# Kernel optimization log

Measured on AMD Instinct MI355X. Metric: run time of the kernel, lower is better.

The kernel has to match this reference:

```python
import jax, jax.numpy as jnp
import numpy as np

N, L, E, NB, H = 128, 200, 128, 2, 2
ITEM = 50000
TEMP = 0.2
HD = E // H


def _ln(x, g, b, eps=1e-8):
    m = x.mean(-1, keepdims=True)
    v = ((x - m) ** 2).mean(-1, keepdims=True)
    return (x - m) / jnp.sqrt(v + eps) * g + b


def setup_inputs() -> dict:
    key = jax.random.key(0)
    ks = jax.random.split(key, 20)
    rng = np.random.default_rng(0)
    log_seqs = rng.integers(1, ITEM + 1, size=(N, L))
    lens = rng.integers(20, L + 1, size=(N,))
    log_seqs[np.arange(L)[None, :] < (L - lens[:, None])] = 0  # left padding, id 0
    pos_seqs = rng.integers(1, ITEM + 1, size=(N, L))
    neg_seqs = rng.integers(1, ITEM + 1, size=(N, L))
    item_emb = jax.random.normal(ks[0], (ITEM + 1, E), jnp.float32) * 0.02
    item_emb = item_emb.at[0].set(0.0)  # padding_idx=0
    s = 1.0 / np.sqrt(E)
    return {
        "item_emb": item_emb,
        "pos_emb": jax.random.normal(ks[1], (L + 1, E), jnp.float32) * 0.02,
        "W_asp": jax.random.normal(ks[2], (16, E, E), jnp.float32) * s,
        "w_weight": jax.random.normal(ks[3], (2 * E,), jnp.float32) * (1.0 / np.sqrt(2 * E)),
        "w_bias": jnp.zeros((), jnp.float32),
        "attn_ln_g": jnp.ones((NB, E), jnp.float32),
        "attn_ln_b": jnp.zeros((NB, E), jnp.float32),
        "in_proj_w": jax.random.normal(ks[4], (NB, 3 * E, E), jnp.float32) * s,
        "in_proj_b": jnp.zeros((NB, 3 * E), jnp.float32),
        "out_proj_w": jax.random.normal(ks[5], (NB, E, E), jnp.float32) * s,
        "out_proj_b": jnp.zeros((NB, E), jnp.float32),
        "fwd_ln_g": jnp.ones((NB, E), jnp.float32),
        "fwd_ln_b": jnp.zeros((NB, E), jnp.float32),
        "conv1_w": jax.random.normal(ks[6], (NB, E, E), jnp.float32) * s,
        "conv1_b": jnp.zeros((NB, E), jnp.float32),
        "conv2_w": jax.random.normal(ks[7], (NB, E, E), jnp.float32) * s,
        "conv2_b": jnp.zeros((NB, E), jnp.float32),
        "last_ln_g": jnp.ones((E,), jnp.float32),
        "last_ln_b": jnp.zeros((E,), jnp.float32),
        "user_ids": jnp.asarray(rng.integers(0, 100000, size=(N,)), jnp.int32),
        "log_seqs": jnp.asarray(log_seqs, jnp.int32),
        "pos_seqs": jnp.asarray(pos_seqs, jnp.int32),
        "neg_seqs": jnp.asarray(neg_seqs, jnp.int32),
        "epoch": 1,
    }


def reference(item_emb, pos_emb, W_asp, w_weight, w_bias, attn_ln_g, attn_ln_b,
              in_proj_w, in_proj_b, out_proj_w, out_proj_b, fwd_ln_g, fwd_ln_b,
              conv1_w, conv1_b, conv2_w, conv2_b, last_ln_g, last_ln_b,
              user_ids, log_seqs, pos_seqs, neg_seqs, epoch):
    tmask = (log_seqs == 0)                               # (N,L) True=pad
    validL = (~tmask).astype(item_emb.dtype)              # (N,L)
    seqs0 = item_emb[log_seqs] * validL[..., None]
    pos_embs = item_emb[pos_seqs] * validL[..., None]
    neg_embs = item_emb[neg_seqs] * validL[..., None]

    validE = jnp.concatenate([validL, validL[:, -1:]], 1)  # (N,L+1)
    kv_save = jnp.concatenate([seqs0, pos_embs[:, -1:, :]], 1)  # (N,L+1,E)

    def aspects(x, valid, residual):
        a = jnp.einsum('nli,aoi->nlao', x, W_asp)          # 16 expert GEMMs batched
        if residual:
            a = a + x[:, :, None, :]
            a = a / (jnp.linalg.norm(a, axis=-1, keepdims=True) + 1e-8)
        return a * valid[:, :, None, None]

    kv4 = aspects(kv_save, validE, True)                   # (N,L+1,16,E)
    temp = aspects(kv_save, validE, False)
    nvalid = validE.sum()
    cent_loss = jnp.linalg.norm(kv_save * validE[..., None] - temp.mean(2), axis=-1).sum() / nvalid

    norm_x = kv4 / (jnp.linalg.norm(kv4, axis=-1, keepdims=True) + 1e-8)
    pos_s = (norm_x * norm_x).sum(-1)                      # (N,L+1,16)
    ttl = jnp.einsum('nlae,nlbe->nlab', norm_x, norm_x)    # pairwise cosine sims
    mi = -(pos_s / TEMP - jnp.log(jnp.exp(ttl / TEMP).sum(-1)))
    ind_loss = (mi * validE[:, :, None]).sum() / nvalid

    s = kv4.sum(2)                                         # (N,L+1,E)
    q = jnp.cumsum(s, 1) - s                               # exclusive cumsum
    cnt = jnp.cumsum(validE, 1) - validE
    q = q / (16.0 * cnt + 1e-8)[..., None] * validE[..., None]

    w_q, w_a = w_weight[:E], w_weight[E:]

    def gate(qv, a4):                                      # learned softmax gating
        logits = (qv @ w_q)[:, :, None] + a4 @ w_a + w_bias
        w = jax.nn.softmax(logits, axis=2)
        return (a4 * w[..., None]).sum(2)

    re_all = gate(q, kv4)                                  # (N,L+1,E)
    re_emb = re_all[:, :L] + kv4[:, :L].mean(2)

    neg_kv4 = aspects(neg_embs, validL, True)
    q2 = q[:, 1:, :] * validL[..., None]
    neg_t = gate(q2, neg_kv4) + neg_kv4.mean(2)
    pos_t = re_all[:, 1:, :] * validL[..., None] + (kv4[:, 1:] * validL[..., None, None]).mean(2)

    seqs = re_emb * (E ** 0.5) + pos_emb[jnp.arange(L)][None]
    seqs = seqs * validL[..., None]
    causal = jnp.where(jnp.tril(jnp.ones((L, L), bool)), 0.0, -1e9)
    scale = HD ** -0.5
    for i in range(NB):
        Qn = _ln(seqs, attn_ln_g[i], attn_ln_b[i])
        qp = Qn @ in_proj_w[i][:E].T + in_proj_b[i][:E]
        kp = seqs @ in_proj_w[i][E:2 * E].T + in_proj_b[i][E:2 * E]
        vp = seqs @ in_proj_w[i][2 * E:].T + in_proj_b[i][2 * E:]
        sp = lambda x: x.reshape(N, L, H, HD).transpose(0, 2, 1, 3)
        att = jax.nn.softmax(jnp.einsum('nhqd,nhkd->nhqk', sp(qp), sp(kp)) * scale + causal, axis=-1)
        o = jnp.einsum('nhqk,nhkd->nhqd', att, sp(vp)).transpose(0, 2, 1, 3).reshape(N, L, E)
        seqs = Qn + (o @ out_proj_w[i].T + out_proj_b[i])
        seqs = _ln(seqs, fwd_ln_g[i], fwd_ln_b[i])
        h = jax.nn.relu(seqs @ conv1_w[i].T + conv1_b[i])
        seqs = (h @ conv2_w[i].T + conv2_b[i]) + seqs
        seqs = seqs * validL[..., None]
    log_feats = _ln(seqs, last_ln_g, last_ln_b)
    pos_logits = (log_feats * pos_t).sum(-1)
    neg_logits = (log_feats * neg_t).sum(-1)
    return (pos_logits, neg_logits, ind_loss, cent_loss)
```

## Files before the change

### kernel.cpp

```cpp
#include <hip/hip_runtime.h>
#include <hip/hip_bf16.h>
#include <cstddef>

typedef __attribute__((ext_vector_type(8))) short bf16x8;
typedef __attribute__((ext_vector_type(4))) float f32x4;
typedef unsigned short ushort_t;

__device__ __forceinline__ short f2bf(float f) {
    __hip_bfloat16 h = __float2bfloat16(f);
    return __builtin_bit_cast(short, h);
}
__device__ __forceinline__ float bf2f(short s) {
    unsigned u = ((unsigned)(unsigned short)s) << 16;
    return __builtin_bit_cast(float, u);
}
__device__ __forceinline__ unsigned pk2(float a, float b) {
    return (unsigned)(unsigned short)f2bf(a) | ((unsigned)(unsigned short)f2bf(b) << 16);
}

__global__ void cvt_all(const float* __restrict__ s0, const float* __restrict__ s1,
                        const float* __restrict__ s2, const float* __restrict__ s3,
                        const float* __restrict__ s4, ushort_t* __restrict__ dst) {
    const int i = blockIdx.x * 256 + threadIdx.x;
    const int mat = i >> 14;
    const int wm = i & 16383;
    const int blk = wm >> 9;
    const int t = blk >> 2, f = blk & 3;
    const int lane = (wm >> 3) & 63;
    const int j = wm & 7;
    const int g4 = lane >> 4, nn = lane & 15;
    const int srcoff = (t * 16 + nn) * 128 + f * 32 + g4 * 8 + j;
    const float* src; int mbase;
    if (mat < 16)      { src = s0; mbase = mat; }
    else if (mat < 22) { src = s1; mbase = mat - 16; }
    else if (mat < 24) { src = s2; mbase = mat - 22; }
    else if (mat < 26) { src = s3; mbase = mat - 24; }
    else               { src = s4; mbase = mat - 26; }
    dst[i] = (ushort_t)f2bf(src[(size_t)mbase * 16384 + srcoff]);
}

__global__ void gather_kernel(const float* __restrict__ item_emb,
                              const int* __restrict__ log_seqs,
                              const int* __restrict__ pos_seqs,
                              const int* __restrict__ neg_seqs,
                              ushort_t* __restrict__ kvx, ushort_t* __restrict__ negx,
                              float* __restrict__ validE, float* __restrict__ validL) {
    const int r = blockIdx.x;
    const int e = threadIdx.x;
    const int NKV = 128 * 201;
    if (r < NKV) {
        const int n = r / 201, l = r % 201;
        float vl; int sidx;
        if (l < 200) { sidx = log_seqs[n * 200 + l]; vl = (sidx != 0) ? 1.f : 0.f; }
        else { vl = (log_seqs[n * 200 + 199] != 0) ? 1.f : 0.f; sidx = pos_seqs[n * 200 + 199]; }
        kvx[(size_t)r * 128 + e] = (ushort_t)f2bf(item_emb[(size_t)sidx * 128 + e] * vl);
        if (e == 0) validE[r] = vl;
    } else {
        const int rr = r - NKV;
        const int n = rr / 200, l = rr % 200;
        const float vl = (log_seqs[n * 200 + l] != 0) ? 1.f : 0.f;
        const int sidx = neg_seqs[n * 200 + l];
        negx[(size_t)rr * 128 + e] = (ushort_t)f2bf(item_emb[(size_t)sidx * 128 + e] * vl);
        if (e == 0) validL[rr] = vl;
    }
}

__global__ __launch_bounds__(512, 1) void aspects2_kernel(
        const ushort_t* __restrict__ X, const ushort_t* __restrict__ Wab,
        const float* __restrict__ w_weight, const float* __restrict__ validf,
        float* __restrict__ Gout, float* __restrict__ pInd, float* __restrict__ pCent,
        int nLossBlocks) {
    __shared__ ushort_t rsb[32 * 2184];
    __shared__ ushort_t xsb[32 * 136];
    __shared__ float wal[128];
    __shared__ float s_red[512];
    __shared__ float s_lg[512];
    __shared__ float s_pos[512];
    __shared__ float vld[32];
    __shared__ float centw[32];
    __shared__ float miw[32];

    const int tid = threadIdx.x;
    const int row0 = blockIdx.x * 32;
    const bool losses = (int)blockIdx.x < nLossBlocks;
    const int lane = tid & 63, w = tid >> 6;
    const int g4 = lane >> 4, nn = lane & 15;

    {
        const int r = tid >> 4, c8 = (tid & 15) * 8;
        *(int4*)&xsb[r * 136 + c8] = *(const int4*)&X[(size_t)(row0 + r) * 128 + c8];
    }
    if (tid < 128) wal[tid] = w_weight[128 + tid];
    if (tid < 32) vld[tid] = validf[row0 + tid];
    __syncthreads();

    bf16x8 xf0[4], xf1[4];
#pragma unroll
    for (int f = 0; f < 4; ++f) {
        xf0[f] = *(const bf16x8*)&xsb[nn * 136 + f * 32 + g4 * 8];
        xf1[f] = *(const bf16x8*)&xsb[(nn + 16) * 136 + f * 32 + g4 * 8];
    }

    for (int al = 0; al < 2; ++al) {
        const int a = w * 2 + al;
        const ushort_t* wbase = Wab + (size_t)a * 16384 + lane * 8;
        float np0 = 0.f, lp0 = 0.f, np1 = 0.f, lp1 = 0.f;
#pragma unroll
        for (int t = 0; t < 8; ++t) {
            f32x4 d0 = {0.f, 0.f, 0.f, 0.f}, d1 = d0;
#pragma unroll
            for (int f = 0; f < 4; ++f) {
                bf16x8 wf = *(const bf16x8*)&wbase[(t * 4 + f) * 512];
                d0 = __builtin_amdgcn_mfma_f32_16x16x32_bf16(wf, xf0[f], d0, 0, 0, 0);
                d1 = __builtin_amdgcn_mfma_f32_16x16x32_bf16(wf, xf1[f], d1, 0, 0, 0);
            }
            const int o0 = t * 16 + g4 * 4;
            const float4 wv = *(const float4*)&wal[o0];
            const int xs0 = o0 & 4;
            {
                const bf16x8 xb = *(const bf16x8*)&xsb[nn * 136 + (o0 & ~7)];
                const float v0 = d0[0] + bf2f(xb[xs0]);
                const float v1 = d0[1] + bf2f(xb[xs0 + 1]);
                const float v2 = d0[2] + bf2f(xb[xs0 + 2]);
                const float v3 = d0[3] + bf2f(xb[xs0 + 3]);
                np0 += v0 * v0 + v1 * v1 + v2 * v2 + v3 * v3;
                lp0 += v0 * wv.x + v1 * wv.y + v2 * wv.z + v3 * wv.w;
                *(int2*)&rsb[nn * 2184 + a * 136 + o0] =
                    make_int2((int)pk2(v0, v1), (int)pk2(v2, v3));
            }
            {
                const bf16x8 xb = *(const bf16x8*)&xsb[(nn + 16) * 136 + (o0 & ~7)];
                const float v0 = d1[0] + bf2f(xb[xs0]);
                const float v1 = d1[1] + bf2f(xb[xs0 + 1]);
                const float v2 = d1[2] + bf2f(xb[xs0 + 2]);
                const float v3 = d1[3] + bf2f(xb[xs0 + 3]);
                np1 += v0 * v0 + v1 * v1 + v2 * v2 + v3 * v3;
                lp1 += v0 * wv.x + v1 * wv.y + v2 * wv.z + v3 * wv.w;
                *(int2*)&rsb[(nn + 16) * 2184 + a * 136 + o0] =
                    make_int2((int)pk2(v0, v1), (int)pk2(v2, v3));
            }
        }
        np0 += __shfl_xor(np0, 16, 64); np0 += __shfl_xor(np0, 32, 64);
        lp0 += __shfl_xor(lp0, 16, 64); lp0 += __shfl_xor(lp0, 32, 64);
        np1 += __shfl_xor(np1, 16, 64); np1 += __shfl_xor(np1, 32, 64);
        lp1 += __shfl_xor(lp1, 16, 64); lp1 += __shfl_xor(lp1, 32, 64);
        if (lane < 16) {
            s_red[nn * 16 + a] = np0;        s_lg[nn * 16 + a] = lp0;
            s_red[(nn + 16) * 16 + a] = np1; s_lg[(nn + 16) * 16 + a] = lp1;
        }
    }
    __syncthreads();

    {
        const float nrm = sqrtf(s_red[tid]);
        const float inv1 = 1.f / (nrm + 1e-8f);
        const float n2 = nrm * inv1;
        const float sg = inv1 / (n2 + 1e-8f);
        const float ts = n2 / (n2 + 1e-8f);
        const float logit = s_lg[tid] * inv1;
        float mx = logit;
#pragma unroll
        for (int m = 1; m < 16; m <<= 1) mx = fmaxf(mx, __shfl_xor(mx, m, 16));
        const float e = __expf(logit - mx);
        float ssum = e;
#pragma unroll
        for (int m = 1; m < 16; m <<= 1) ssum += __shfl_xor(ssum, m, 16);
        s_red[tid] = sg;
        s_pos[tid] = ts * ts * 5.f;
        s_lg[tid] = (e / ssum + 0.0625f) * inv1;
    }
    __syncthreads();

    {
        const int row = tid >> 4, ol = tid & 15, o8 = ol * 8;
        float g[8] = {0.f, 0.f, 0.f, 0.f, 0.f, 0.f, 0.f, 0.f};
        float sr[8] = {0.f, 0.f, 0.f, 0.f, 0.f, 0.f, 0.f, 0.f};
#pragma unroll
        for (int a = 0; a < 16; ++a) {
            const bf16x8 vb = *(const bf16x8*)&rsb[row * 2184 + a * 136 + o8];
            const float gw = s_lg[row * 16 + a];
#pragma unroll
            for (int j = 0; j < 8; ++j) {
                const float v = bf2f(vb[j]);
                g[j] += v * gw;
                if (losses) sr[j] += v;
            }
        }
        float* go = &Gout[(size_t)(row0 + row) * 128 + o8];
        *(float4*)go       = make_float4(g[0], g[1], g[2], g[3]);
        *(float4*)(go + 4) = make_float4(g[4], g[5], g[6], g[7]);
        if (losses) {
            const bf16x8 xb = *(const bf16x8*)&xsb[row * 136 + o8];
            float c = 0.f;
#pragma unroll
            for (int j = 0; j < 8; ++j) {
                const float dd = 2.f * bf2f(xb[j]) - sr[j] * 0.0625f;
                c += dd * dd;
            }
            c += __shfl_xor(c, 1, 64);
            c += __shfl_xor(c, 2, 64);
            c += __shfl_xor(c, 4, 64);
            c += __shfl_xor(c, 8, 64);
            if (ol == 0) centw[row] = sqrtf(c) * vld[row];
        }
    }

    if (losses) {
        for (int rl = 0; rl < 4; ++rl) {
            const int row = w * 4 + rl;
            f32x4 dd = {0.f, 0.f, 0.f, 0.f};
#pragma unroll
            for (int f = 0; f < 4; ++f) {
                bf16x8 fr = *(const bf16x8*)&rsb[row * 2184 + nn * 136 + f * 32 + g4 * 8];
                dd = __builtin_amdgcn_mfma_f32_16x16x32_bf16(fr, fr, dd, 0, 0, 0);
            }
            const float sgb = s_red[row * 16 + nn];
            float mis = 0.f;
#pragma unroll
            for (int r = 0; r < 4; ++r) {
                const int a = g4 * 4 + r;
                const float sga = s_red[row * 16 + a];
                float eb = __expf(5.f * dd[r] * sga * sgb);
#pragma unroll
                for (int m = 1; m < 16; m <<= 1) eb += __shfl_xor(eb, m, 16);
                mis += -(s_pos[row * 16 + a] - logf(eb));
            }
            mis += __shfl_xor(mis, 16, 64);
            mis += __shfl_xor(mis, 32, 64);
            if (lane == 0) miw[row] = mis * vld[row];
        }
        __syncthreads();
        if (tid == 0) {
            float si = 0.f, sc = 0.f;
#pragma unroll
            for (int r = 0; r < 32; ++r) { si += miw[r]; sc += centw[r]; }
            pInd[blockIdx.x] = si;
            pCent[blockIdx.x] = sc;
        }
    }
}

__global__ __launch_bounds__(256) void qkv_kernel(const float* __restrict__ X,
                                                  const ushort_t* __restrict__ W3,
                                                  const float* __restrict__ b3,
                                                  const float* __restrict__ lng,
                                                  const float* __restrict__ lnb,
                                                  float* __restrict__ Xn,
                                                  ushort_t* __restrict__ qo,
                                                  ushort_t* __restrict__ ko,
                                                  ushort_t* __restrict__ vo) {
    const int tid = threadIdx.x, lane = tid & 63, w = tid >> 6;
    const int q = lane >> 4, nn = lane & 15;
    const int m0 = blockIdx.x * 64 + w * 16;
    float xv[4][8];
    float s = 0.f, sq = 0.f;
    const float* xr = &X[(size_t)(m0 + nn) * 128];
#pragma unroll
    for (int f = 0; f < 4; ++f) {
        const float4 a = *(const float4*)&xr[f * 32 + q * 8];
        const float4 b = *(const float4*)&xr[f * 32 + q * 8 + 4];
        xv[f][0] = a.x; xv[f][1] = a.y; xv[f][2] = a.z; xv[f][3] = a.w;
        xv[f][4] = b.x; xv[f][5] = b.y; xv[f][6] = b.z; xv[f][7] = b.w;
        s += (a.x + a.y) + (a.z + a.w) + (b.x + b.y) + (b.z + b.w);
        sq += (a.x * a.x + a.y * a.y) + (a.z * a.z + a.w * a.w)
            + (b.x * b.x + b.y * b.y) + (b.z * b.z + b.w * b.w);
    }
    bf16x8 afr[4];
#pragma unroll
    for (int f = 0; f < 4; ++f) {
        bf16x8 v;
#pragma unroll
        for (int j = 0; j < 8; ++j) v[j] = f2bf(xv[f][j]);
        afr[f] = v;
    }
    s += __shfl_xor(s, 16, 64);  s += __shfl_xor(s, 32, 64);
    sq += __shfl_xor(sq, 16, 64); sq += __shfl_xor(sq, 32, 64);
    const float mean = s * 0.0078125f;
    const float var = fmaxf(sq * 0.0078125f - mean * mean, 0.f);
    const float inv = rsqrtf(var + 1e-8f);
    bf16x8 afq[4];
#pragma unroll
    for (int f = 0; f < 4; ++f) {
        const int c0 = f * 32 + q * 8;
        const float4 ga = *(const float4*)&lng[c0];
        const float4 gb = *(const float4*)&lng[c0 + 4];
        const float4 ba = *(const float4*)&lnb[c0];
        const float4 bb = *(const float4*)&lnb[c0 + 4];
        float y[8];
        y[0] = (xv[f][0] - mean) * inv * ga.x + ba.x;
        y[1] = (xv[f][1] - mean) * inv * ga.y + ba.y;
        y[2] = (xv[f][2] - mean) * inv * ga.z + ba.z;
        y[3] = (xv[f][3] - mean) * inv * ga.w + ba.w;
        y[4] = (xv[f][4] - mean) * inv * gb.x + bb.x;
        y[5] = (xv[f][5] - mean) * inv * gb.y + bb.y;
        y[6] = (xv[f][6] - mean) * inv * gb.z + bb.z;
        y[7] = (xv[f][7] - mean) * inv * gb.w + bb.w;
        float* xo = &Xn[(size_t)(m0 + nn) * 128 + c0];
        *(float4*)xo       = make_float4(y[0], y[1], y[2], y[3]);
        *(float4*)(xo + 4) = make_float4(y[4], y[5], y[6], y[7]);
        bf16x8 v;
#pragma unroll
        for (int j = 0; j < 8; ++j) v[j] = f2bf(y[j]);
        afq[f] = v;
    }
    ushort_t* const outs[3] = {qo, ko, vo};
#pragma unroll
    for (int mi = 0; mi < 3; ++mi) {
        const ushort_t* wbase = W3 + (size_t)mi * 16384 + lane * 8;
        f32x4 acc[8];
#pragma unroll
        for (int t = 0; t < 8; ++t) acc[t] = (f32x4){0.f, 0.f, 0.f, 0.f};
#pragma unroll
        for (int t = 0; t < 8; ++t) {
#pragma unroll
            for (int f = 0; f < 4; ++f) {
                bf16x8 b = *(const bf16x8*)&wbase[(t * 4 + f) * 512];
                acc[t] = __builtin_amdgcn_mfma_f32_16x16x32_bf16(
                    (mi == 0) ? afq[f] : afr[f], b, acc[t], 0, 0, 0);
            }
        }
        const float* bi = b3 + mi * 128;
        ushort_t* outp = outs[mi];
#pragma unroll
        for (int t = 0; t < 8; ++t) {
            const int n = t * 16 + nn;
            const float bv = bi[n];
#pragma unroll
            for (int r = 0; r < 4; ++r) {
                const int row = m0 + q * 4 + r;
                outp[(size_t)row * 128 + n] = (ushort_t)f2bf(acc[t][r] + bv);
            }
        }
    }
}

__global__ __launch_bounds__(256) void ffn_kernel(const ushort_t* __restrict__ attno,
                                                  const ushort_t* __restrict__ outWb,
                                                  const float* __restrict__ outB,
                                                  const float* __restrict__ resQn,
                                                  const float* __restrict__ lng,
                                                  const float* __restrict__ lnb,
                                                  const ushort_t* __restrict__ c1wb,
                                                  const float* __restrict__ c1b,
                                                  const ushort_t* __restrict__ c2wb,
                                                  const float* __restrict__ c2b,
                                                  const float* __restrict__ validL,
                                                  float* __restrict__ seqs) {
    __shared__ ushort_t hls[64 * 136];
    const int tid = threadIdx.x, lane = tid & 63, w = tid >> 6;
    const int q = lane >> 4, nn = lane & 15;
    const int m0 = blockIdx.x * 64 + w * 16;
    const int wrow = w * 16;

    bf16x8 af[4];
    {
        const ushort_t* xb = &attno[(size_t)(m0 + nn) * 128];
#pragma unroll
        for (int f = 0; f < 4; ++f) af[f] = *(const bf16x8*)&xb[f * 32 + q * 8];
    }
    f32x4 acc[8];
#pragma unroll
    for (int t = 0; t < 8; ++t) acc[t] = (f32x4){0.f, 0.f, 0.f, 0.f};
    {
        const ushort_t* wbase = outWb + lane * 8;
#pragma unroll
        for (int t = 0; t < 8; ++t)
#pragma unroll
            for (int f = 0; f < 4; ++f) {
                bf16x8 b = *(const bf16x8*)&wbase[(t * 4 + f) * 512];
                acc[t] = __builtin_amdgcn_mfma_f32_16x16x32_bf16(af[f], b, acc[t], 0, 0, 0);
            }
    }
    float y[8][4];
    float s[4] = {0.f, 0.f, 0.f, 0.f}, sq[4] = {0.f, 0.f, 0.f, 0.f};
#pragma unroll
    for (int t = 0; t < 8; ++t) {
        const int n = t * 16 + nn;
        const float bi = outB[n];
#pragma unroll
        for (int r = 0; r < 4; ++r) {
            const float v = acc[t][r] + bi + resQn[(size_t)(m0 + q * 4 + r) * 128 + n];
            y[t][r] = v;
            s[r] += v;
            sq[r] += v * v;
        }
    }
#pragma unroll
    for (int m = 1; m < 16; m <<= 1) {
#pragma unroll
        for (int r = 0; r < 4; ++r) {
            s[r] += __shfl_xor(s[r], m, 64);
            sq[r] += __shfl_xor(sq[r], m, 64);
        }
    }
#pragma unroll
    for (int r = 0; r < 4; ++r) {
        const float mean = s[r] * 0.0078125f;
        const float var = fmaxf(sq[r] * 0.0078125f - mean * mean, 0.f);
        const float inv = rsqrtf(var + 1e-8f);
        s[r] = mean; sq[r] = inv;
    }
#pragma unroll
    for (int t = 0; t < 8; ++t) {
        const int n = t * 16 + nn;
        const float g = lng[n], b = lnb[n];
#pragma unroll
        for (int r = 0; r < 4; ++r) {
            const float v = (y[t][r] - s[r]) * sq[r] * g + b;
            y[t][r] = v;
            hls[(wrow + q * 4 + r) * 136 + n] = (ushort_t)f2bf(v);
        }
    }
    __syncthreads();
    {
        const ushort_t* xb = &hls[(wrow + nn) * 136];
#pragma unroll
        for (int f = 0; f < 4; ++f) af[f] = *(const bf16x8*)&xb[f * 32 + q * 8];
    }
    f32x4 acc2[8];
#pragma unroll
    for (int t = 0; t < 8; ++t) acc2[t] = (f32x4){0.f, 0.f, 0.f, 0.f};
    {
        const ushort_t* wbase = c1wb + lane * 8;
#pragma unroll
        for (int t = 0; t < 8; ++t)
#pragma unroll
            for (int f = 0; f < 4; ++f) {
                bf16x8 b = *(const bf16x8*)&wbase[(t * 4 + f) * 512];
                acc2[t] = __builtin_amdgcn_mfma_f32_16x16x32_bf16(af[f], b, acc2[t], 0, 0, 0);
            }
    }
    __syncthreads();
#pragma unroll
    for (int t = 0; t < 8; ++t) {
        const int n = t * 16 + nn;
        const float bi = c1b[n];
#pragma unroll
        for (int r = 0; r < 4; ++r)
            hls[(wrow + q * 4 + r) * 136 + n] = (ushort_t)f2bf(fmaxf(acc2[t][r] + bi, 0.f));
    }
    __syncthreads();
    {
        const ushort_t* xb = &hls[(wrow + nn) * 136];
#pragma unroll
        for (int f = 0; f < 4; ++f) af[f] = *(const bf16x8*)&xb[f * 32 + q * 8];
    }
    f32x4 acc3[8];
#pragma unroll
    for (int t = 0; t < 8; ++t) acc3[t] = (f32x4){0.f, 0.f, 0.f, 0.f};
    {
        const ushort_t* wbase = c2wb + lane * 8;
#pragma unroll
        for (int t = 0; t < 8; ++t)
#pragma unroll
            for (int f = 0; f < 4; ++f) {
                bf16x8 b = *(const bf16x8*)&wbase[(t * 4 + f) * 512];
                acc3[t] = __builtin_amdgcn_mfma_f32_16x16x32_bf16(af[f], b, acc3[t], 0, 0, 0);
            }
    }
    float mk[4];
#pragma unroll
    for (int r = 0; r < 4; ++r) mk[r] = validL[m0 + q * 4 + r];
#pragma unroll
    for (int t = 0; t < 8; ++t) {
        const int n = t * 16 + nn;
        const float bi = c2b[n];
#pragma unroll
        for (int r = 0; r < 4; ++r) {
            const int row = m0 + q * 4 + r;
            seqs[(size_t)row * 128 + n] = (acc3[t][r] + bi + y[t][r]) * mk[r];
        }
    }
}

__global__ void reduce_kernel(const float* __restrict__ pInd, const float* __restrict__ pCent,
                              int nblk, const float* __restrict__ validE, int nve,
                              float* __restrict__ outp) {
    __shared__ float a1[256], a2[256], a3[256];
    const int tid = threadIdx.x;
    float si = 0.f, sc = 0.f, nv = 0.f;
    for (int t = tid; t < nblk; t += 256) { si += pInd[t]; sc += pCent[t]; }
    for (int t = tid; t < nve; t += 256) nv += validE[t];
    a1[tid] = si; a2[tid] = sc; a3[tid] = nv;
    __syncthreads();
    for (int s = 128; s > 0; s >>= 1) {
        if (tid < s) { a1[tid] += a1[tid + s]; a2[tid] += a2[tid + s]; a3[tid] += a3[tid + s]; }
        __syncthreads();
    }
    if (tid == 0) { outp[0] = a1[0] / a3[0]; outp[1] = a2[0] / a3[0]; }
}

__global__ void seqs_init(const float* __restrict__ G, const float* __restrict__ pos_emb,
                          const float* __restrict__ validL, float* __restrict__ seqs) {
    const int idx = blockIdx.x * 256 + threadIdx.x;
    const int e = idx & 127;
    const int nl = idx >> 7;
    const int l = nl % 200, n = nl / 200;
    const float v = G[((size_t)n * 201 + l) * 128 + e] * 11.313708498984761f + pos_emb[l * 128 + e];
    seqs[idx] = v * validL[nl];
}

__global__ __launch_bounds__(256) void attn_kernel(const ushort_t* __restrict__ qp,
                                                   const ushort_t* __restrict__ kp,
                                                   const ushort_t* __restrict__ vp,
                                                   ushort_t* __restrict__ outp) {
    __shared__ ushort_t KsU[2048];
    __shared__ ushort_t VtU[2560];
    __shared__ ushort_t Pb[2560];

    const int tid = threadIdx.x, lane = tid & 63, w = tid >> 6;
    const int b = blockIdx.x;
    const int nh = b >> 2, qt = b & 3;
    const int n = nh >> 1, h = nh & 1;
    const size_t base = (size_t)n * 200 * 128 + (size_t)h * 64;
    const int qw = qt * 64 + w * 16;
    const bool wactive = qw < 200;
    const int q15 = lane & 15, g4 = lane >> 4;
    const int qglob = qw + q15;

    bf16x8 qf[2];
    {
        const int qr = (qglob < 200) ? qglob : 199;
#pragma unroll
        for (int f = 0; f < 2; ++f)
            qf[f] = *(const bf16x8*)&qp[base + (size_t)qr * 128 + f * 32 + g4 * 8];
    }
    f32x4 Oacc[4];
#pragma unroll
    for (int nt = 0; nt < 4; ++nt) Oacc[nt] = (f32x4){0.f, 0.f, 0.f, 0.f};
    float mrun = -1e30f, lrun = 0.f;

    const int kmax = min(200, qt * 64 + 64);
    ushort_t* PbW = Pb + w * 640;

    for (int jt = 0; jt < kmax; jt += 32) {
        __syncthreads();
        {
            const int k = tid >> 3, e0 = (tid & 7) * 8;
            const int krow = jt + k;
            int4 a = make_int4(0, 0, 0, 0);
            if (krow < 200) a = *(const int4*)&kp[base + (size_t)krow * 128 + e0];
            *(int4*)&KsU[(k * 128 + ((e0 * 2) ^ ((k & 7) << 4))) >> 1] = a;
        }
        {
            const int k = tid & 31, e0 = (tid >> 5) * 8;
            const int vrow = jt + k;
            int4 a = make_int4(0, 0, 0, 0);
            if (vrow < 200) a = *(const int4*)&vp[base + (size_t)vrow * 128 + e0];
            VtU[(e0 + 0) * 40 + k] = (ushort_t)((unsigned)a.x & 0xFFFF);
            VtU[(e0 + 1) * 40 + k] = (ushort_t)((unsigned)a.x >> 16);
            VtU[(e0 + 2) * 40 + k] = (ushort_t)((unsigned)a.y & 0xFFFF);
            VtU[(e0 + 3) * 40 + k] = (ushort_t)((unsigned)a.y >> 16);
            VtU[(e0 + 4) * 40 + k] = (ushort_t)((unsigned)a.z & 0xFFFF);
            VtU[(e0 + 5) * 40 + k] = (ushort_t)((unsigned)a.z >> 16);
            VtU[(e0 + 6) * 40 + k] = (ushort_t)((unsigned)a.w & 0xFFFF);
            VtU[(e0 + 7) * 40 + k] = (ushort_t)((unsigned)a.w >> 16);
        }
        __syncthreads();
        if (!wactive) continue;

        f32x4 d0 = {0.f, 0.f, 0.f, 0.f}, d1 = d0;
#pragma unroll
        for (int f = 0; f < 2; ++f) {
            const int ebyte = g4 * 16 + f * 64;
            const int sw = ebyte ^ ((q15 & 7) << 4);
            bf16x8 a0 = *(const bf16x8*)&KsU[(q15 * 128 + sw) >> 1];
            bf16x8 a1 = *(const bf16x8*)&KsU[((q15 + 16) * 128 + sw) >> 1];
            d0 = __builtin_amdgcn_mfma_f32_16x16x32_bf16(a0, qf[f], d0, 0, 0, 0);
            d1 = __builtin_amdgcn_mfma_f32_16x16x32_bf16(a1, qf[f], d1, 0, 0, 0);
        }
        const int kb = jt + g4 * 4;
        float p[8];
        float tmax = -1e30f;
#pragma unroll
        for (int r = 0; r < 4; ++r) {
            const float s0 = (kb + r      <= qglob) ? d0[r] * 0.125f : -1e30f;
            const float s1 = (kb + r + 16 <= qglob) ? d1[r] * 0.125f : -1e30f;
            p[r] = s0; p[r + 4] = s1;
            tmax = fmaxf(tmax, fmaxf(s0, s1));
        }
        tmax = fmaxf(tmax, __shfl_xor(tmax, 16, 64));
        tmax = fmaxf(tmax, __shfl_xor(tmax, 32, 64));
        const float mnew = fmaxf(mrun, tmax);
        const float corr = __expf(mrun - mnew);
        mrun = mnew;
        float tsum = 0.f;
#pragma unroll
        for (int i = 0; i < 8; ++i) {
            float pe = __expf(p[i] - mnew);
            pe = bf2f(f2bf(pe));
            p[i] = pe;
            tsum += pe;
        }
        tsum += __shfl_xor(tsum, 16, 64);
        tsum += __shfl_xor(tsum, 32, 64);
        lrun = lrun * corr + tsum;
        const int kl = g4 * 4;
        *(unsigned*)&PbW[q15 * 40 + kl]          = pk2(p[0], p[1]);
        *(unsigned*)&PbW[q15 * 40 + kl + 2]      = pk2(p[2], p[3]);
        *(unsigned*)&PbW[q15 * 40 + 16 + kl]     = pk2(p[4], p[5]);
        *(unsigned*)&PbW[q15 * 40 + 16 + kl + 2] = pk2(p[6], p[7]);
        asm volatile("" ::: "memory");
        float corr_r[4];
#pragma unroll
        for (int r = 0; r < 4; ++r) corr_r[r] = __shfl(corr, g4 * 4 + r, 64);
#pragma unroll
        for (int nt = 0; nt < 4; ++nt) {
#pragma unroll
            for (int r = 0; r < 4; ++r) Oacc[nt][r] *= corr_r[r];
        }
        bf16x8 pa = *(const bf16x8*)&PbW[q15 * 40 + g4 * 8];
#pragma unroll
        for (int nt = 0; nt < 4; ++nt) {
            bf16x8 vb = *(const bf16x8*)&VtU[(nt * 16 + q15) * 40 + g4 * 8];
            Oacc[nt] = __builtin_amdgcn_mfma_f32_16x16x32_bf16(pa, vb, Oacc[nt], 0, 0, 0);
        }
    }
    if (wactive) {
        float linv[4];
#pragma unroll
        for (int r = 0; r < 4; ++r) linv[r] = 1.f / __shfl(lrun, g4 * 4 + r, 64);
#pragma unroll
        for (int r = 0; r < 4; ++r) {
            const int qg = qw + g4 * 4 + r;
            if (qg < 200) {
#pragma unroll
                for (int nt = 0; nt < 4; ++nt)
                    outp[base + (size_t)qg * 128 + nt * 16 + q15] =
                        (ushort_t)f2bf(Oacc[nt][r] * linv[r]);
            }
        }
    }
}

__global__ __launch_bounds__(256) void logits_kernel(const float* __restrict__ seqs,
                                                     const float* __restrict__ lastg,
                                                     const float* __restrict__ lastb,
                                                     const float* __restrict__ G,
                                                     const float* __restrict__ negt,
                                                     const float* __restrict__ validL,
                                                     float* __restrict__ outp) {
    const int row = blockIdx.x * 4 + (threadIdx.x >> 6);
    const int lane = threadIdx.x & 63;
    if (row >= 25600) return;
    const int n = row / 200, j = row % 200;
    const float2 x = *(const float2*)&seqs[(size_t)row * 128 + lane * 2];
    float s = x.x + x.y, sq = x.x * x.x + x.y * x.y;
#pragma unroll
    for (int m = 1; m < 64; m <<= 1) { s += __shfl_xor(s, m, 64); sq += __shfl_xor(sq, m, 64); }
    const float mean = s * 0.0078125f;
    const float var = fmaxf(sq * 0.0078125f - mean * mean, 0.f);
    const float inv = rsqrtf(var + 1e-8f);
    const float2 gg = *(const float2*)&lastg[lane * 2];
    const float2 bb = *(const float2*)&lastb[lane * 2];
    const float y0 = (x.x - mean) * inv * gg.x + bb.x;
    const float y1 = (x.y - mean) * inv * gg.y + bb.y;
    const float2 g2 = *(const float2*)&G[((size_t)n * 201 + j + 1) * 128 + lane * 2];
    const float2 t2 = *(const float2*)&negt[(size_t)row * 128 + lane * 2];
    float sp = y0 * g2.x + y1 * g2.y;
    float sn = y0 * t2.x + y1 * t2.y;
#pragma unroll
    for (int m = 1; m < 64; m <<= 1) { sp += __shfl_xor(sp, m, 64); sn += __shfl_xor(sn, m, 64); }
    if (lane == 0) { outp[row] = sp * validL[row]; outp[25600 + row] = sn; }
}

extern "C" void kernel_launch(void* const* d_in, const int* in_sizes, int n_in,
                              void* d_out, int out_size, void* d_ws, size_t ws_size,
                              hipStream_t stream) {
    (void)in_sizes; (void)n_in; (void)out_size; (void)ws_size;
    const float* item_emb = (const float*)d_in[0];
    const float* pos_emb  = (const float*)d_in[1];
    const float* W_asp    = (const float*)d_in[2];
    const float* w_weight = (const float*)d_in[3];
    const float* attn_g = (const float*)d_in[5];
    const float* attn_b = (const float*)d_in[6];
    const float* inW    = (const float*)d_in[7];
    const float* inB    = (const float*)d_in[8];
    const float* outW   = (const float*)d_in[9];
    const float* outB   = (const float*)d_in[10];
    const float* fwd_g  = (const float*)d_in[11];
    const float* fwd_b  = (const float*)d_in[12];
    const float* c1w    = (const float*)d_in[13];
    const float* c1b    = (const float*)d_in[14];
    const float* c2w    = (const float*)d_in[15];
    const float* c2b    = (const float*)d_in[16];
    const float* last_g = (const float*)d_in[17];
    const float* last_b = (const float*)d_in[18];
    const int* log_seqs = (const int*)d_in[20];
    const int* pos_seqs = (const int*)d_in[21];
    const int* neg_seqs = (const int*)d_in[22];

    float* ws = (float*)d_ws;
    const size_t S = (size_t)128 * 201 * 128;
    ushort_t* kvx  = (ushort_t*)ws;
    ushort_t* negx = kvx + S;
    ushort_t* qp = (ushort_t*)ws;
    ushort_t* kp = qp + (size_t)25600 * 128;
    float* G     = ws + 2 * S;
    float* negt  = ws + 3 * S;
    float* seqs  = ws + 4 * S;
    float* Qn    = ws + 5 * S;
    ushort_t* vp    = (ushort_t*)(ws + 6 * S);
    ushort_t* attno = (ushort_t*)(ws + 7 * S);
    ushort_t* wb  = (ushort_t*)(ws + 8 * S);
    ushort_t* Wab  = wb;
    ushort_t* inWb = Wab + 262144;
    ushort_t* outWb = inWb + 98304;
    ushort_t* c1b_w = outWb + 32768;
    ushort_t* c2b_w = c1b_w + 32768;
    float* validE = ws + 8 * S + 229376;
    float* validL = validE + 128 * 201;
    float* pInd   = validL + 128 * 200;
    float* pCent  = pInd + 804;
    float* outF   = (float*)d_out;

    cvt_all<<<dim3(1792), dim3(256), 0, stream>>>(W_asp, inW, outW, c1w, c2w, wb);
    gather_kernel<<<dim3(128 * 201 + 128 * 200), dim3(128), 0, stream>>>(
        item_emb, log_seqs, pos_seqs, neg_seqs, kvx, negx, validE, validL);
    aspects2_kernel<<<dim3(1604), dim3(512), 0, stream>>>(
        kvx, Wab, w_weight, validE, G, pInd, pCent, 804);
    reduce_kernel<<<dim3(1), dim3(256), 0, stream>>>(
        pInd, pCent, 804, validE, 128 * 201, outF + 51200);
    seqs_init<<<dim3(12800), dim3(256), 0, stream>>>(G, pos_emb, validL, seqs);

    for (int i = 0; i < 2; ++i) {
        qkv_kernel<<<dim3(400), dim3(256), 0, stream>>>(
            seqs, inWb + (size_t)i * 3 * 16384, inB + (size_t)i * 384,
            attn_g + i * 128, attn_b + i * 128, Qn, qp, kp, vp);
        attn_kernel<<<dim3(1024), dim3(256), 0, stream>>>(qp, kp, vp, attno);
        ffn_kernel<<<dim3(400), dim3(256), 0, stream>>>(
            attno, outWb + (size_t)i * 16384, outB + i * 128, Qn,
            fwd_g + i * 128, fwd_b + i * 128,
            c1b_w + (size_t)i * 16384, c1b + i * 128,
            c2b_w + (size_t)i * 16384, c2b + i * 128,
            validL, seqs);
    }
    logits_kernel<<<dim3(6400), dim3(256), 0, stream>>>(
        seqs, last_g, last_b, G, negt, validL, outF);
}
```

Measured before the change: 243.9 us.

## Fuse seqs init into aspects kernel and compute norms/logits via MFMA Gram

Removes the separate seqs_init launch by writing the scaled G plus positional embedding directly from the aspects kernel for the loss blocks, which cover the KV rows. Replaces the per-thread norm and logit accumulation in the aspect loop with an MFMA pass over the stored bf16 aspect results: the Gram diagonal gives the norms and a product with bf16 w_weight gives the logits. The Gram is then reused for the later MI loss instead of being recomputed. This cuts one kernel launch and a global read/write of seqs, but norms and logits are now computed from bf16-rounded values.

Result: faster. 232.0 us (-4.9%).

```diff
diff --git a/kernel.cpp b/kernel.cpp
--- a/kernel.cpp
+++ b/kernel.cpp
@@ -68,11 +68,13 @@
 __global__ __launch_bounds__(512, 1) void aspects2_kernel(
         const ushort_t* __restrict__ X, const ushort_t* __restrict__ Wab,
         const float* __restrict__ w_weight, const float* __restrict__ validf,
-        float* __restrict__ Gout, float* __restrict__ pInd, float* __restrict__ pCent,
+        const float* __restrict__ pos_emb,
+        float* __restrict__ Gout, float* __restrict__ seqs,
+        float* __restrict__ pInd, float* __restrict__ pCent,
         int nLossBlocks) {
     __shared__ ushort_t rsb[32 * 2184];
     __shared__ ushort_t xsb[32 * 136];
-    __shared__ float wal[128];
+    __shared__ ushort_t wal_b[128];
     __shared__ float s_red[512];
     __shared__ float s_lg[512];
     __shared__ float s_pos[512];
@@ -90,21 +92,21 @@
         const int r = tid >> 4, c8 = (tid & 15) * 8;
         *(int4*)&xsb[r * 136 + c8] = *(const int4*)&X[(size_t)(row0 + r) * 128 + c8];
     }
-    if (tid < 128) wal[tid] = w_weight[128 + tid];
+    if (tid < 128) wal_b[tid] = (ushort_t)f2bf(w_weight[128 + tid]);
     if (tid < 32) vld[tid] = validf[row0 + tid];
     __syncthreads();
 
-    bf16x8 xf0[4], xf1[4];
+    bf16x8 xf0[4], xf1[4], waf[4];
 #pragma unroll
     for (int f = 0; f < 4; ++f) {
         xf0[f] = *(const bf16x8*)&xsb[nn * 136 + f * 32 + g4 * 8];
         xf1[f] = *(const bf16x8*)&xsb[(nn + 16) * 136 + f * 32 + g4 * 8];
+        waf[f] = *(const bf16x8*)&wal_b[f * 32 + g4 * 8];
     }
 
     for (int al = 0; al < 2; ++al) {
         const int a = w * 2 + al;
         const ushort_t* wbase = Wab + (size_t)a * 16384 + lane * 8;
-        float np0 = 0.f, lp0 = 0.f, np1 = 0.f, lp1 = 0.f;
 #pragma unroll
         for (int t = 0; t < 8; ++t) {
             f32x4 d0 = {0.f, 0.f, 0.f, 0.f}, d1 = d0;
@@ -115,38 +117,40 @@
                 d1 = __builtin_amdgcn_mfma_f32_16x16x32_bf16(wf, xf1[f], d1, 0, 0, 0);
             }
             const int o0 = t * 16 + g4 * 4;
-            const float4 wv = *(const float4*)&wal[o0];
             const int xs0 = o0 & 4;
             {
                 const bf16x8 xb = *(const bf16x8*)&xsb[nn * 136 + (o0 & ~7)];
-                const float v0 = d0[0] + bf2f(xb[xs0]);
-                const float v1 = d0[1] + bf2f(xb[xs0 + 1]);
-                const float v2 = d0[2] + bf2f(xb[xs0 + 2]);
-                const float v3 = d0[3] + bf2f(xb[xs0 + 3]);
-                np0 += v0 * v0 + v1 * v1 + v2 * v2 + v3 * v3;
-                lp0 += v0 * wv.x + v1 * wv.y + v2 * wv.z + v3 * wv.w;
-                *(int2*)&rsb[nn * 2184 + a * 136 + o0] =
-                    make_int2((int)pk2(v0, v1), (int)pk2(v2, v3));
+                *(int2*)&rsb[nn * 2184 + a * 136 + o0] = make_int2(
+                    (int)pk2(d0[0] + bf2f(xb[xs0]),     d0[1] + bf2f(xb[xs0 + 1])),
+                    (int)pk2(d0[2] + bf2f(xb[xs0 + 2]), d0[3] + bf2f(xb[xs0 + 3])));
             }
             {
                 const bf16x8 xb = *(const bf16x8*)&xsb[(nn + 16) * 136 + (o0 & ~7)];
-                const float v0 = d1[0] + bf2f(xb[xs0]);
-                const float v1 = d1[1] + bf2f(xb[xs0 + 1]);
-                const float v2 = d1[2] + bf2f(xb[xs0 + 2]);
-                const float v3 = d1[3] + bf2f(xb[xs0 + 3]);
-                np1 += v0 * v0 + v1 * v1 + v2 * v2 + v3 * v3;
-                lp1 += v0 * wv.x + v1 * wv.y + v2 * wv.z + v3 * wv.w;
-                *(int2*)&rsb[(nn + 16) * 2184 + a * 136 + o0] =
-                    make_int2((int)pk2(v0, v1), (int)pk2(v2, v3));
-            }
-        }
-        np0 += __shfl_xor(np0, 16, 64); np0 += __shfl_xor(np0, 32, 64);
-        lp0 += __shfl_xor(lp0, 16, 64); lp0 += __shfl_xor(lp0, 32, 64);
-        np1 += __shfl_xor(np1, 16, 64); np1 += __shfl_xor(np1, 32, 64);
-        lp1 += __shfl_xor(lp1, 16, 64); lp1 += __shfl_xor(lp1, 32, 64);
-        if (lane < 16) {
-            s_red[nn * 16 + a] = np0;        s_lg[nn * 16 + a] = lp0;
-            s_red[(nn + 16) * 16 + a] = np1; s_lg[(nn + 16) * 16 + a] = lp1;
+                *(int2*)&rsb[(nn + 16) * 2184 + a * 136 + o0] = make_int2(
+                    (int)pk2(d1[0] + bf2f(xb[xs0]),     d1[1] + bf2f(xb[xs0 + 1])),
+                    (int)pk2(d1[2] + bf2f(xb[xs0 + 2]), d1[3] + bf2f(xb[xs0 + 3])));
+            }
+        }
+    }
+    __syncthreads();
+
+    f32x4 gram0 = {0.f,0.f,0.f,0.f}, gram1 = gram0, gram2 = gram0, gram3 = gram0;
+#pragma unroll
+    for (int rl = 0; rl < 4; ++rl) {
+        const int row = w * 4 + rl;
+        f32x4 dgr = {0.f, 0.f, 0.f, 0.f}, dlp = dgr;
+#pragma unroll
+        for (int f = 0; f < 4; ++f) {
+            bf16x8 fr = *(const bf16x8*)&rsb[row * 2184 + nn * 136 + f * 32 + g4 * 8];
+            dgr = __builtin_amdgcn_mfma_f32_16x16x32_bf16(fr, fr, dgr, 0, 0, 0);
+            dlp = __builtin_amdgcn_mfma_f32_16x16x32_bf16(fr, waf[f], dlp, 0, 0, 0);
+        }
+        if (rl == 0) gram0 = dgr; else if (rl == 1) gram1 = dgr;
+        else if (rl == 2) gram2 = dgr; else gram3 = dgr;
+        if (g4 == (nn >> 2)) s_red[row * 16 + nn] = dgr[nn & 3];
+        if (nn == 0) {
+#pragma unroll
+            for (int r = 0; r < 4; ++r) s_lg[row * 16 + g4 * 4 + r] = dlp[r];
         }
     }
     __syncthreads();
@@ -190,6 +194,19 @@
         *(float4*)go       = make_float4(g[0], g[1], g[2], g[3]);
         *(float4*)(go + 4) = make_float4(g[4], g[5], g[6], g[7]);
         if (losses) {
+            const int rg = row0 + row;
+            const int nq = rg / 201, l = rg % 201;
+            if (l < 200) {
+                const float4 p0 = *(const float4*)&pos_emb[l * 128 + o8];
+                const float4 p1 = *(const float4*)&pos_emb[l * 128 + o8 + 4];
+                const float vv = vld[row];
+                float* so = &seqs[(size_t)(nq * 200 + l) * 128 + o8];
+                const float SQ = 11.313708498984761f;
+                *(float4*)so = make_float4((g[0] * SQ + p0.x) * vv, (g[1] * SQ + p0.y) * vv,
+                                           (g[2] * SQ + p0.z) * vv, (g[3] * SQ + p0.w) * vv);
+                *(float4*)(so + 4) = make_float4((g[4] * SQ + p1.x) * vv, (g[5] * SQ + p1.y) * vv,
+                                                 (g[6] * SQ + p1.z) * vv, (g[7] * SQ + p1.w) * vv);
+            }
             const bf16x8 xb = *(const bf16x8*)&xsb[row * 136 + o8];
             float c = 0.f;
 #pragma unroll
@@ -206,14 +223,10 @@
     }
 
     if (losses) {
+#pragma unroll
         for (int rl = 0; rl < 4; ++rl) {
             const int row = w * 4 + rl;
-            f32x4 dd = {0.f, 0.f, 0.f, 0.f};
-#pragma unroll
-            for (int f = 0; f < 4; ++f) {
-                bf16x8 fr = *(const bf16x8*)&rsb[row * 2184 + nn * 136 + f * 32 + g4 * 8];
-                dd = __builtin_amdgcn_mfma_f32_16x16x32_bf16(fr, fr, dd, 0, 0, 0);
-            }
+            const f32x4 dd = (rl == 0) ? gram0 : (rl == 1) ? gram1 : (rl == 2) ? gram2 : gram3;
             const float sgb = s_red[row * 16 + nn];
             float mis = 0.f;
 #pragma unroll
@@ -488,16 +501,6 @@
         __syncthreads();
     }
     if (tid == 0) { outp[0] = a1[0] / a3[0]; outp[1] = a2[0] / a3[0]; }
-}
-
-__global__ void seqs_init(const float* __restrict__ G, const float* __restrict__ pos_emb,
-                          const float* __restrict__ validL, float* __restrict__ seqs) {
-    const int idx = blockIdx.x * 256 + threadIdx.x;
-    const int e = idx & 127;
-    const int nl = idx >> 7;
-    const int l = nl % 200, n = nl / 200;
-    const float v = G[((size_t)n * 201 + l) * 128 + e] * 11.313708498984761f + pos_emb[l * 128 + e];
-    seqs[idx] = v * validL[nl];
 }
 
 __global__ __launch_bounds__(256) void attn_kernel(const ushort_t* __restrict__ qp,
@@ -718,10 +721,9 @@
     gather_kernel<<<dim3(128 * 201 + 128 * 200), dim3(128), 0, stream>>>(
         item_emb, log_seqs, pos_seqs, neg_seqs, kvx, negx, validE, validL);
     aspects2_kernel<<<dim3(1604), dim3(512), 0, stream>>>(
-        kvx, Wab, w_weight, validE, G, pInd, pCent, 804);
+        kvx, Wab, w_weight, validE, pos_emb, G, seqs, pInd, pCent, 804);
     reduce_kernel<<<dim3(1), dim3(256), 0, stream>>>(
         pInd, pCent, 804, validE, 128 * 201, outF + 51200);
-    seqs_init<<<dim3(12800), dim3(256), 0, stream>>>(G, pos_emb, validL, seqs);
 
     for (int i = 0; i < 2; ++i) {
         qkv_kernel<<<dim3(400), dim3(256), 0, stream>>>(
```
